# Optimization experiments

Hardware: AMD Instinct MI355X
Metric: run time of the kernel (lower is better)

The kernel has to match this reference:

```python
import jax, jax.numpy as jnp
import numpy as np

B, S, D, H, W = 8, 2048, 128, 8, 64
INT_HEADS = 8          # hardcoded in SpatioTemporalLayer1
EPS_COS = 1e-8
EPS_LN = 1e-5


def _mha(q_in, k_in, v_in, in_w, in_b, out_w, out_b, nh, mask=None):
    # q_in/k_in/v_in: (batch, len, d); torch nn.MultiheadAttention math (eval, no dropout)
    b, lq, d = q_in.shape
    hd = d // nh
    q = (q_in @ in_w[:d].T + in_b[:d]).reshape(b, lq, nh, hd)
    k = (k_in @ in_w[d:2 * d].T + in_b[d:2 * d]).reshape(b, k_in.shape[1], nh, hd)
    v = (v_in @ in_w[2 * d:].T + in_b[2 * d:]).reshape(b, v_in.shape[1], nh, hd)
    scores = jnp.einsum('bihd,bjhd->bhij', q, k) / jnp.sqrt(jnp.asarray(hd, q_in.dtype))
    if mask is not None:
        scores = scores + mask
    attn = jax.nn.softmax(scores, axis=-1)
    out = jnp.einsum('bhij,bjhd->bihd', attn, v).reshape(b, lq, d)
    return out @ out_w.T + out_b


def _layernorm(x, g, b):
    mu = x.mean(-1, keepdims=True)
    var = ((x - mu) ** 2).mean(-1, keepdims=True)
    return (x - mu) * jax.lax.rsqrt(var + EPS_LN) * g + b


def _cos_normalize(e):
    n = jnp.maximum(jnp.linalg.norm(e, axis=-1, keepdims=True), EPS_COS)
    return e / n


def _forward(x, spatial_info, temporal_info,
             lw_in_w, lw_in_b, lw_out_w, lw_out_b,
             spat_w, spat_b, temp_w, temp_b,
             int_in_w, int_in_b, int_out_w, int_out_b,
             ffn_w1, ffn_b1, ffn_w2, ffn_b2,
             ln1_g, ln1_b, ln2_g, ln2_b):
    b, s, d = x.shape
    # --- local window attention (S % W == 0 here, so no padding path) ---
    nw = s // W
    xw = x.reshape(b * nw, W, d)
    causal = jnp.triu(jnp.full((W, W), -jnp.inf, x.dtype), k=1)
    attn = _mha(xw, xw, xw, lw_in_w, lw_in_b, lw_out_w, lw_out_b, H, causal).reshape(b, s, d)
    x = _layernorm(attn + x, ln1_g, ln1_b)
    # --- FFN (torch nn.GELU default = exact erf) ---
    h = jax.nn.gelu(x @ ffn_w1.T + ffn_b1, approximate=False)
    x = _layernorm(h @ ffn_w2.T + ffn_b2 + x, ln2_g, ln2_b)
    # --- spatio-temporal interaction ---
    se = spatial_info @ spat_w.T + spat_b
    te = temporal_info @ temp_w.T + temp_b
    sn = _cos_normalize(se)
    tn = _cos_normalize(te)
    ss = jnp.einsum('bid,bjd->bij', sn, sn)   # (B,S,S) spatial cosine sim
    ts = jnp.einsum('bid,bjd->bij', tn, tn)   # (B,S,S) temporal cosine sim
    # interaction MHA is batch_first=False: it treats (B,S,D) as (len=B, batch=S, d).
    # Equivalent batch-first call on swapped axes (faithful to the torch source).
    inter = jnp.swapaxes(
        _mha(jnp.swapaxes(se, 0, 1), jnp.swapaxes(te, 0, 1), jnp.swapaxes(te, 0, 1),
             int_in_w, int_in_b, int_out_w, int_out_b, INT_HEADS), 0, 1)
    # similarity[b,i,j,d] = ss[b,i,j]*ts[b,i,j]*inter[b,i,d]; mean over j factorizes:
    sim = (ss * ts).mean(axis=2)              # (B,S)
    return x + sim[..., None] * inter


def setup_inputs() -> dict:
    key = jax.random.key(0)
    ks = jax.random.split(key, 24)
    sc = 0.02
    inp = {
        'x': jax.random.normal(ks[0], (B, S, D), jnp.float32),
        'spatial_info': jax.random.normal(ks[1], (B, S, D), jnp.float32),
        'temporal_info': jax.random.normal(ks[2], (B, S, D), jnp.float32),
        'lw_in_w': jax.random.normal(ks[3], (3 * D, D), jnp.float32) * sc,
        'lw_in_b': jnp.zeros((3 * D,), jnp.float32),
        'lw_out_w': jax.random.normal(ks[4], (D, D), jnp.float32) * sc,
        'lw_out_b': jnp.zeros((D,), jnp.float32),
        'spat_w': jax.random.normal(ks[5], (D, D), jnp.float32) * sc,
        'spat_b': jnp.zeros((D,), jnp.float32),
        'temp_w': jax.random.normal(ks[6], (D, D), jnp.float32) * sc,
        'temp_b': jnp.zeros((D,), jnp.float32),
        'int_in_w': jax.random.normal(ks[7], (3 * D, D), jnp.float32) * sc,
        'int_in_b': jnp.zeros((3 * D,), jnp.float32),
        'int_out_w': jax.random.normal(ks[8], (D, D), jnp.float32) * sc,
        'int_out_b': jnp.zeros((D,), jnp.float32),
        'ffn_w1': jax.random.normal(ks[9], (4 * D, D), jnp.float32) * sc,
        'ffn_b1': jnp.zeros((4 * D,), jnp.float32),
        'ffn_w2': jax.random.normal(ks[10], (D, 4 * D), jnp.float32) * sc,
        'ffn_b2': jnp.zeros((D,), jnp.float32),
        'ln1_g': jnp.ones((D,), jnp.float32),
        'ln1_b': jnp.zeros((D,), jnp.float32),
        'ln2_g': jnp.ones((D,), jnp.float32),
        'ln2_b': jnp.zeros((D,), jnp.float32),
    }
    return inp


def reference(x, spatial_info, temporal_info,
              lw_in_w, lw_in_b, lw_out_w, lw_out_b,
              spat_w, spat_b, temp_w, temp_b,
              int_in_w, int_in_b, int_out_w, int_out_b,
              ffn_w1, ffn_b1, ffn_w2, ffn_b2,
              ln1_g, ln1_b, ln2_g, ln2_b):
    return _forward(x, spatial_info, temporal_info,
                    lw_in_w, lw_in_b, lw_out_w, lw_out_b,
                    spat_w, spat_b, temp_w, temp_b,
                    int_in_w, int_in_b, int_out_w, int_out_b,
                    ffn_w1, ffn_b1, ffn_w2, ffn_b2,
                    ln1_g, ln1_b, ln2_g, ln2_b)
```

## Files before the change

### kernel.cpp

```cpp
#include <hip/hip_runtime.h>
#include <math.h>

#define BB 8
#define SS 2048
#define NTOK (BB * SS)

using bf16x8 = __attribute__((ext_vector_type(8))) short;
using f32x4  = __attribute__((ext_vector_type(4))) float;

__device__ __forceinline__ float gelu_tanh(float x) {
    float y = 0.7978845608f * (x + 0.044715f * x * x * x);
    float e = __expf(2.0f * y);
    float t = 1.0f - 2.0f / (e + 1.0f);
    return 0.5f * x * (1.0f + t);
}
__device__ __forceinline__ unsigned short f2b(float f) {
    unsigned int u = __float_as_uint(f);
    u += 0x7FFFu + ((u >> 16) & 1u);
    return (unsigned short)(u >> 16);
}
__device__ __forceinline__ float b2f(unsigned short u) {
    return __uint_as_float((unsigned int)u << 16);
}
__device__ __forceinline__ bf16x8 ldg_f32_b8(const float* p) {
    float4 f0 = *(const float4*)p, f1 = *(const float4*)(p + 4);
    union { ushort4 u[2]; bf16x8 v; } r;
    r.u[0] = (ushort4){f2b(f0.x), f2b(f0.y), f2b(f0.z), f2b(f0.w)};
    r.u[1] = (ushort4){f2b(f1.x), f2b(f1.y), f2b(f1.z), f2b(f1.w)};
    return r.v;
}

__global__ __launch_bounds__(256) void phase0(
    const float* __restrict__ x,
    const float* __restrict__ lw_in_w, const float* __restrict__ b_in,
    const float* __restrict__ lw_out_w,
    const float* __restrict__ spat_w, const float* __restrict__ temp_w,
    const float* __restrict__ ffn_w1, const float* __restrict__ ffn_w2,
    const float* __restrict__ int_in_w, const float* __restrict__ int_out_w,
    const float* __restrict__ spatial, const float* __restrict__ temporal,
    unsigned short* __restrict__ Wlwob, unsigned short* __restrict__ Wstb,
    unsigned short* __restrict__ Wb,
    unsigned short* __restrict__ Wib, unsigned short* __restrict__ Wiob,
    unsigned short* __restrict__ spb, unsigned short* __restrict__ tpb,
    unsigned short* __restrict__ qkvb,
    float* __restrict__ Mf)
{
    const int tid = threadIdx.x;
    if (blockIdx.x < 256) {
        const int m0 = blockIdx.x * 64;
        const int wv = tid >> 6, lane = tid & 63, ln = lane & 15, q = lane >> 4;
        const int wm = (wv >> 1) * 32, wn = (wv & 1) * 64;
        bf16x8 afr[4][2];
        #pragma unroll
        for (int kf = 0; kf < 4; ++kf)
            #pragma unroll
            for (int fm = 0; fm < 2; ++fm)
                afr[kf][fm] = ldg_f32_b8(x + (size_t)(m0 + wm + fm * 16 + ln) * 128 + kf * 32 + q * 8);
        #pragma unroll
        for (int p = 0; p < 3; ++p) {
            f32x4 acc[2][4] = {};
            #pragma unroll
            for (int kf = 0; kf < 4; ++kf) {
                bf16x8 b[4];
                #pragma unroll
                for (int fn = 0; fn < 4; ++fn)
                    b[fn] = ldg_f32_b8(lw_in_w + (size_t)(p * 128 + wn + fn * 16 + ln) * 128 + kf * 32 + q * 8);
                #pragma unroll
                for (int fm = 0; fm < 2; ++fm)
                    #pragma unroll
                    for (int fn = 0; fn < 4; ++fn)
                        acc[fm][fn] = __builtin_amdgcn_mfma_f32_16x16x32_bf16(afr[kf][fm], b[fn], acc[fm][fn], 0, 0, 0);
            }
            #pragma unroll
            for (int fm = 0; fm < 2; ++fm)
                #pragma unroll
                for (int r = 0; r < 4; ++r) {
                    int rl = wm + fm * 16 + q * 4 + r;
                    #pragma unroll
                    for (int fn = 0; fn < 4; ++fn) {
                        int col = wn + fn * 16 + ln;
                        qkvb[(size_t)(m0 + rl) * 384 + p * 128 + col] =
                            f2b(acc[fm][fn][r] + b_in[p * 128 + col]);
                    }
                }
        }
        return;
    }
    int v = (blockIdx.x - 256) * 256 + tid;
    if (v < 61440) {
        const float* src; unsigned short* dst; int off;
        if (v < 4096)       { src = lw_out_w;  dst = Wlwob;         off = v; }
        else if (v < 8192)  { src = spat_w;    dst = Wstb;          off = v - 4096; }
        else if (v < 12288) { src = temp_w;    dst = Wstb + 16384;  off = v - 8192; }
        else if (v < 28672) { src = ffn_w1;    dst = Wb;            off = v - 12288; }
        else if (v < 45056) { src = ffn_w2;    dst = Wb + 65536;    off = v - 28672; }
        else if (v < 57344) { src = int_in_w;  dst = Wib;           off = v - 45056; }
        else                { src = int_out_w; dst = Wiob;          off = v - 57344; }
        float4 f = *(const float4*)(src + (size_t)off * 4);
        *(ushort4*)(dst + (size_t)off * 4) =
            (ushort4){f2b(f.x), f2b(f.y), f2b(f.z), f2b(f.w)};
    } else if (v < 94208) {
        *(float4*)(Mf + (size_t)(v - 61440) * 4) = (float4){0.f, 0.f, 0.f, 0.f};
    } else {
        int u = v - 94208;
        const float* src; unsigned short* dst;
        if (u < 524288) { src = spatial;  dst = spb; }
        else            { src = temporal; dst = tpb; u -= 524288; }
        float4 f = *(const float4*)(src + (size_t)u * 4);
        *(ushort4*)(dst + (size_t)u * 4) =
            (ushort4){f2b(f.x), f2b(f.y), f2b(f.z), f2b(f.w)};
    }
}

__global__ __launch_bounds__(256) void phase1(
    const float* __restrict__ x,
    const unsigned short* __restrict__ qkvb,
    const unsigned short* __restrict__ lwoutb,
    const float* __restrict__ b_out,
    const float* __restrict__ lng, const float* __restrict__ lnb,
    float* __restrict__ x1, unsigned short* __restrict__ x1b,
    const unsigned short* __restrict__ spb, const unsigned short* __restrict__ tpb,
    const unsigned short* __restrict__ spwb, const unsigned short* __restrict__ tpwb,
    const float* __restrict__ bsp, const float* __restrict__ btp,
    unsigned short* __restrict__ snb, unsigned short* __restrict__ tnb,
    unsigned short* __restrict__ seb, unsigned short* __restrict__ teb)
{
    __shared__ unsigned short Qs[64 * 136];
    __shared__ unsigned short Ks[64 * 136];
    __shared__ unsigned short Vt[128 * 72];
    __shared__ unsigned short Pb[4][32 * 72];
    __shared__ float red[2][128][2];
    const int tid = threadIdx.x;
    const int wv = tid >> 6, lane = tid & 63, ln = lane & 15, q = lane >> 4;

    if (blockIdx.x >= 256) {
        const int idx2 = blockIdx.x - 256;
        const int y = idx2 >> 7;
        const int m0 = (idx2 & 127) * 128;
        const unsigned short* Ab = y ? tpb : spb;
        const unsigned short* Wfb = y ? tpwb : spwb;
        const float* bias = y ? btp : bsp;
        unsigned short* nb = y ? tnb : snb;
        unsigned short* raw = y ? teb : seb;
        const int wm = (wv >> 1) * 64, wn = (wv & 1) * 64;

        f32x4 acc[4][4] = {};
        #pragma unroll
        for (int kf = 0; kf < 4; ++kf) {
            bf16x8 a[4], b[4];
            #pragma unroll
            for (int fm = 0; fm < 4; ++fm)
                a[fm] = *(const bf16x8*)&Ab[(size_t)(m0 + wm + fm * 16 + ln) * 128 + kf * 32 + q * 8];
            #pragma unroll
            for (int fn = 0; fn < 4; ++fn)
                b[fn] = *(const bf16x8*)&Wfb[(size_t)(wn + fn * 16 + ln) * 128 + kf * 32 + q * 8];
            #pragma unroll
            for (int fm = 0; fm < 4; ++fm)
                #pragma unroll
                for (int fn = 0; fn < 4; ++fn)
                    acc[fm][fn] = __builtin_amdgcn_mfma_f32_16x16x32_bf16(a[fm], b[fn], acc[fm][fn], 0, 0, 0);
        }
        #pragma unroll
        for (int fm = 0; fm < 4; ++fm)
            #pragma unroll
            for (int r = 0; r < 4; ++r) {
                int rl = wm + fm * 16 + q * 4 + r;
                float s2 = 0.0f;
                #pragma unroll
                for (int fn = 0; fn < 4; ++fn) {
                    int col = wn + fn * 16 + ln;
                    float vv = acc[fm][fn][r] + bias[col];
                    acc[fm][fn][r] = vv;
                    s2 += vv * vv;
                }
                #pragma unroll
                for (int off = 1; off < 16; off <<= 1) s2 += __shfl_xor(s2, off, 64);
                if (ln == 0) red[0][rl][wv & 1] = s2;
            }
        __syncthreads();
        #pragma unroll
        for (int fm = 0; fm < 4; ++fm)
            #pragma unroll
            for (int r = 0; r < 4; ++r) {
                int rl = wm + fm * 16 + q * 4 + r;
                int row = m0 + rl;
                float inv = 1.0f / fmaxf(sqrtf(red[0][rl][0] + red[0][rl][1]), 1e-8f);
                #pragma unroll
                for (int fn = 0; fn < 4; ++fn) {
                    int col = wn + fn * 16 + ln;
                    float vv = acc[fm][fn][r];
                    nb[(size_t)row * 128 + col] = f2b(vv * inv);
                    raw[(size_t)row * 128 + col] = f2b(vv);
                }
            }
        return;
    }

    const int m0 = blockIdx.x * 64;
    const int wm = (wv >> 1) * 32, wn = (wv & 1) * 64;

    {
        const unsigned short* qrow = qkvb + (size_t)m0 * 384;
        #pragma unroll
        for (int t = 0; t < 12; ++t) {
            int idx = tid + t * 256;
            int r = idx / 48, c = (idx % 48) * 8;
            uint4 vv = *(const uint4*)&qrow[(size_t)r * 384 + c];
            if (c < 128)      *(uint4*)&Qs[r * 136 + c] = vv;
            else if (c < 256) *(uint4*)&Ks[r * 136 + (c - 128)] = vv;
            else {
                const unsigned short* pv = (const unsigned short*)&vv;
                #pragma unroll
                for (int c2 = 0; c2 < 8; ++c2)
                    Vt[(c - 256 + c2) * 72 + r] = pv[c2];
            }
        }
    }
    __syncthreads();

    {
        const int mh = wv >> 1, hq = wv & 1;
        unsigned short* P = &Pb[wv][0];
        #pragma unroll
        for (int hh = 0; hh < 4; ++hh) {
            const int h = hq * 4 + hh;
            f32x4 sacc[2][4] = {};
            bf16x8 az[2] = {}, bz[4] = {};
            if (q < 2) {
                #pragma unroll
                for (int fm = 0; fm < 2; ++fm)
                    az[fm] = *(const bf16x8*)&Qs[(mh * 32 + fm * 16 + ln) * 136 + h * 16 + q * 8];
                #pragma unroll
                for (int fn = 0; fn < 4; ++fn)
                    bz[fn] = *(const bf16x8*)&Ks[(fn * 16 + ln) * 136 + h * 16 + q * 8];
            }
            #pragma unroll
            for (int fm = 0; fm < 2; ++fm)
                #pragma unroll
                for (int fn = 0; fn < 4; ++fn)
                    sacc[fm][fn] = __builtin_amdgcn_mfma_f32_16x16x32_bf16(az[fm], bz[fn], sacc[fm][fn], 0, 0, 0);
            float invr[2][4];
            #pragma unroll
            for (int fm = 0; fm < 2; ++fm)
                #pragma unroll
                for (int r = 0; r < 4; ++r) {
                    int gi = mh * 32 + fm * 16 + q * 4 + r;
                    float mx = -1e30f;
                    #pragma unroll
                    for (int fn = 0; fn < 4; ++fn) {
                        int j = fn * 16 + ln;
                        float s = sacc[fm][fn][r] * 0.25f;
                        if (j > gi) s = -1e30f;
                        sacc[fm][fn][r] = s;
                        mx = fmaxf(mx, s);
                    }
                    #pragma unroll
                    for (int off = 1; off < 16; off <<= 1)
                        mx = fmaxf(mx, __shfl_xor(mx, off, 64));
                    float sum = 0.0f;
                    #pragma unroll
                    for (int fn = 0; fn < 4; ++fn) {
                        float p_ = __expf(sacc[fm][fn][r] - mx);
                        sacc[fm][fn][r] = p_;
                        sum += p_;
                    }
                    #pragma unroll
                    for (int off = 1; off < 16; off <<= 1)
                        sum += __shfl_xor(sum, off, 64);
                    invr[fm][r] = 1.0f / sum;
                    #pragma unroll
                    for (int fn = 0; fn < 4; ++fn)
                        P[(fm * 16 + q * 4 + r) * 72 + fn * 16 + ln] = f2b(sacc[fm][fn][r]);
                }
            f32x4 oacc[2] = {};
            #pragma unroll
            for (int kf2 = 0; kf2 < 2; ++kf2) {
                bf16x8 pa[2], vb;
                #pragma unroll
                for (int fm = 0; fm < 2; ++fm)
                    pa[fm] = *(const bf16x8*)&P[(fm * 16 + ln) * 72 + kf2 * 32 + q * 8];
                vb = *(const bf16x8*)&Vt[(h * 16 + ln) * 72 + kf2 * 32 + q * 8];
                #pragma unroll
                for (int fm = 0; fm < 2; ++fm)
                    oacc[fm] = __builtin_amdgcn_mfma_f32_16x16x32_bf16(pa[fm], vb, oacc[fm], 0, 0, 0);
            }
            #pragma unroll
            for (int fm = 0; fm < 2; ++fm)
                #pragma unroll
                for (int r = 0; r < 4; ++r)
                    Qs[(mh * 32 + fm * 16 + q * 4 + r) * 136 + h * 16 + ln] =
                        f2b(oacc[fm][r] * invr[fm][r]);
        }
    }
    __syncthreads();

    f32x4 acc[2][4] = {};
    #pragma unroll
    for (int kf = 0; kf < 4; ++kf) {
        bf16x8 a[2], b[4];
        #pragma unroll
        for (int fm = 0; fm < 2; ++fm)
            a[fm] = *(const bf16x8*)&Qs[(wm + fm * 16 + ln) * 136 + kf * 32 + q * 8];
        #pragma unroll
        for (int fn = 0; fn < 4; ++fn)
            b[fn] = *(const bf16x8*)&lwoutb[(size_t)(wn + fn * 16 + ln) * 128 + kf * 32 + q * 8];
        #pragma unroll
        for (int fm = 0; fm < 2; ++fm)
            #pragma unroll
            for (int fn = 0; fn < 4; ++fn)
                acc[fm][fn] = __builtin_amdgcn_mfma_f32_16x16x32_bf16(a[fm], b[fn], acc[fm][fn], 0, 0, 0);
    }
    #pragma unroll
    for (int fm = 0; fm < 2; ++fm)
        #pragma unroll
        for (int r = 0; r < 4; ++r) {
            int rl = wm + fm * 16 + q * 4 + r;
            int row = m0 + rl;
            float s1 = 0.0f, s2 = 0.0f;
            #pragma unroll
            for (int fn = 0; fn < 4; ++fn) {
                int col = wn + fn * 16 + ln;
                float vv = acc[fm][fn][r] + b_out[col] + x[(size_t)row * 128 + col];
                acc[fm][fn][r] = vv;
                s1 += vv; s2 += vv * vv;
            }
            #pragma unroll
            for (int off = 1; off < 16; off <<= 1) {
                s1 += __shfl_xor(s1, off, 64);
                s2 += __shfl_xor(s2, off, 64);
            }
            if (ln == 0) { red[0][rl][wv & 1] = s1; red[1][rl][wv & 1] = s2; }
        }
    __syncthreads();
    #pragma unroll
    for (int fm = 0; fm < 2; ++fm)
        #pragma unroll
        for (int r = 0; r < 4; ++r) {
            int rl = wm + fm * 16 + q * 4 + r;
            int row = m0 + rl;
            float mu = (red[0][rl][0] + red[0][rl][1]) * (1.0f / 128.0f);
            float var = (red[1][rl][0] + red[1][rl][1]) * (1.0f / 128.0f) - mu * mu;
            float rs = rsqrtf(var + 1e-5f);
            #pragma unroll
            for (int fn = 0; fn < 4; ++fn) {
                int col = wn + fn * 16 + ln;
                float o = (acc[fm][fn][r] - mu) * rs * lng[col] + lnb[col];
                x1[(size_t)row * 128 + col] = o;
                x1b[(size_t)row * 128 + col] = f2b(o);
            }
        }
}

__global__ __launch_bounds__(256) void phase2(
    const unsigned short* __restrict__ x1b, const float* __restrict__ x1,
    const unsigned short* __restrict__ Wb,
    const float* __restrict__ b1, const float* __restrict__ b2,
    const float* __restrict__ lng, const float* __restrict__ lnb,
    float* __restrict__ x2,
    const unsigned short* __restrict__ snb, const unsigned short* __restrict__ tnb,
    float* __restrict__ Mf)
{
    __shared__ __align__(16) char pool[34816];
    const int tid = threadIdx.x;
    const int wv = tid >> 6, lane = tid & 63, ln = lane & 15, q = lane >> 4;

    if (blockIdx.x < 512) {
        unsigned short* Hw = (unsigned short*)pool + wv * 1152;
        float* part = (float*)(pool + 9216);
        const int t0 = blockIdx.x * 32;
        const int rg = wv & 1, hh = wv >> 1;
        const int r0 = t0 + rg * 16;
        const unsigned short* w1 = Wb;
        const unsigned short* w2 = Wb + 65536;

        bf16x8 afr[4];
        #pragma unroll
        for (int kf = 0; kf < 4; ++kf)
            afr[kf] = *(const bf16x8*)&x1b[(size_t)(r0 + ln) * 128 + kf * 32 + q * 8];

        f32x4 acc2[8] = {};
        #pragma unroll
        for (int ch = 0; ch < 4; ++ch) {
            const int hc0 = (hh * 4 + ch) * 64;
            f32x4 acc1[4] = {};
            #pragma unroll
            for (int kf = 0; kf < 4; ++kf) {
                bf16x8 b[4];
                #pragma unroll
                for (int fn = 0; fn < 4; ++fn)
                    b[fn] = *(const bf16x8*)&w1[(size_t)(hc0 + fn * 16 + ln) * 128 + kf * 32 + q * 8];
                #pragma unroll
                for (int fn = 0; fn < 4; ++fn)
                    acc1[fn] = __builtin_amdgcn_mfma_f32_16x16x32_bf16(afr[kf], b[fn], acc1[fn], 0, 0, 0);
            }
            #pragma unroll
            for (int fn = 0; fn < 4; ++fn)
                #pragma unroll
                for (int r = 0; r < 4; ++r)
                    Hw[(q * 4 + r) * 72 + fn * 16 + ln] =
                        f2b(gelu_tanh(acc1[fn][r] + b1[hc0 + fn * 16 + ln]));
            #pragma unroll
            for (int kf2 = 0; kf2 < 2; ++kf2) {
                bf16x8 a = *(const bf16x8*)&Hw[ln * 72 + kf2 * 32 + q * 8];
                bf16x8 b8[8];
                #pragma unroll
                for (int fn = 0; fn < 8; ++fn)
                    b8[fn] = *(const bf16x8*)&w2[(size_t)(fn * 16 + ln) * 512 + hc0 + kf2 * 32 + q * 8];
                #pragma unroll
                for (int fn = 0; fn < 8; ++fn)
                    acc2[fn] = __builtin_amdgcn_mfma_f32_16x16x32_bf16(a, b8[fn], acc2[fn], 0, 0, 0);
            }
        }
        float* pw = part + rg * 2112;
        if (hh == 1) {
            #pragma unroll
            for (int fn = 0; fn < 8; ++fn)
                #pragma unroll
                for (int r = 0; r < 4; ++r)
                    pw[(q * 4 + r) * 132 + fn * 16 + ln] = acc2[fn][r];
        }
        __syncthreads();
        if (hh == 1) return;
        #pragma unroll
        for (int r = 0; r < 4; ++r) {
            int row = r0 + q * 4 + r;
            float s1 = 0.0f, s2 = 0.0f;
            #pragma unroll
            for (int fn = 0; fn < 8; ++fn) {
                int col = fn * 16 + ln;
                float vv = acc2[fn][r] + pw[(q * 4 + r) * 132 + col]
                         + b2[col] + x1[(size_t)row * 128 + col];
                acc2[fn][r] = vv;
                s1 += vv; s2 += vv * vv;
            }
            #pragma unroll
            for (int off = 1; off < 16; off <<= 1) {
                s1 += __shfl_xor(s1, off, 64);
                s2 += __shfl_xor(s2, off, 64);
            }
            float mu = s1 * (1.0f / 128.0f);
            float var = s2 * (1.0f / 128.0f) - mu * mu;
            float rs = rsqrtf(var + 1e-5f);
            #pragma unroll
            for (int fn = 0; fn < 8; ++fn) {
                int col = fn * 16 + ln;
                x2[(size_t)row * 128 + col] = (acc2[fn][r] - mu) * rs * lng[col] + lnb[col];
            }
        }
        return;
    }

    {
        unsigned short* Sst = (unsigned short*)pool;
        unsigned short* Tst = (unsigned short*)(pool + 17408);
        const int idx2 = blockIdx.x - 512;
        const int d0 = (idx2 & 1) * 64, e0 = ((idx2 >> 1) & 1) * 64;
        const int z = idx2 >> 2;
        const int b = z >> 4, chunk = z & 15;
        const size_t rowb = (size_t)(b * SS + chunk * 128);

        #pragma unroll
        for (int it = 0; it < 4; ++it) {
            int j = (tid & 31) + it * 32;
            int c8 = (tid >> 5) * 8;
            uint4 sv = *(const uint4*)&snb[(rowb + j) * 128 + d0 + c8];
            uint4 tv = *(const uint4*)&tnb[(rowb + j) * 128 + e0 + c8];
            const unsigned short* sp = (const unsigned short*)&sv;
            const unsigned short* tp = (const unsigned short*)&tv;
            #pragma unroll
            for (int c = 0; c < 8; ++c) {
                Sst[(c8 + c) * 136 + j] = sp[c];
                Tst[(c8 + c) * 136 + j] = tp[c];
            }
        }
        __syncthreads();

        const int wm = (wv >> 1) * 32, wn = (wv & 1) * 32;
        f32x4 acc[2][2] = {};
        #pragma unroll
        for (int kf = 0; kf < 4; ++kf) {
            bf16x8 a[2], bb[2];
            #pragma unroll
            for (int fm = 0; fm < 2; ++fm)
                a[fm] = *(const bf16x8*)&Tst[(wm + fm * 16 + ln) * 136 + kf * 32 + q * 8];
            #pragma unroll
            for (int fn = 0; fn < 2; ++fn)
                bb[fn] = *(const bf16x8*)&Sst[(wn + fn * 16 + ln) * 136 + kf * 32 + q * 8];
            #pragma unroll
            for (int fm = 0; fm < 2; ++fm)
                #pragma unroll
                for (int fn = 0; fn < 2; ++fn)
                    acc[fm][fn] = __builtin_amdgcn_mfma_f32_16x16x32_bf16(a[fm], bb[fn], acc[fm][fn], 0, 0, 0);
        }
        float* pp = Mf + (size_t)b * 16384;
        #pragma unroll
        for (int fm = 0; fm < 2; ++fm)
            #pragma unroll
            for (int r = 0; r < 4; ++r) {
                int ee = e0 + wm + fm * 16 + q * 4 + r;
                #pragma unroll
                for (int fn = 0; fn < 2; ++fn) {
                    int dd = d0 + wn + fn * 16 + ln;
                    unsafeAtomicAdd(&pp[(size_t)ee * 128 + dd], acc[fm][fn][r]);
                }
            }
    }
}

__global__ __launch_bounds__(256) void simgemm_kernel(
    const unsigned short* __restrict__ snb, const unsigned short* __restrict__ tnb,
    const float* __restrict__ Mf, float* __restrict__ sim)
{
    __shared__ float red[64][2];
    const int tid = threadIdx.x, m0 = blockIdx.x * 64, b = m0 >> 11;
    const int wv = tid >> 6, lane = tid & 63, ln = lane & 15, q = lane >> 4;
    const int wm = (wv >> 1) * 32, wn = (wv & 1) * 64;

    f32x4 acc[2][4] = {};
    #pragma unroll
    for (int kf = 0; kf < 4; ++kf) {
        bf16x8 a[2], bb[4];
        #pragma unroll
        for (int fm = 0; fm < 2; ++fm)
            a[fm] = *(const bf16x8*)&snb[(size_t)(m0 + wm + fm * 16 + ln) * 128 + kf * 32 + q * 8];
        #pragma unroll
        for (int fn = 0; fn < 4; ++fn)
            bb[fn] = ldg_f32_b8(Mf + (size_t)b * 16384 + (size_t)(wn + fn * 16 + ln) * 128 + kf * 32 + q * 8);
        #pragma unroll
        for (int fm = 0; fm < 2; ++fm)
            #pragma unroll
            for (int fn = 0; fn < 4; ++fn)
                acc[fm][fn] = __builtin_amdgcn_mfma_f32_16x16x32_bf16(a[fm], bb[fn], acc[fm][fn], 0, 0, 0);
    }
    #pragma unroll
    for (int fm = 0; fm < 2; ++fm)
        #pragma unroll
        for (int r = 0; r < 4; ++r) {
            int rl = wm + fm * 16 + q * 4 + r;
            int row = m0 + rl;
            float s = 0.0f;
            #pragma unroll
            for (int fn = 0; fn < 4; ++fn) {
                int col = wn + fn * 16 + ln;
                s += acc[fm][fn][r] * b2f(tnb[(size_t)row * 128 + col]);
            }
            #pragma unroll
            for (int off = 1; off < 16; off <<= 1) s += __shfl_xor(s, off, 64);
            if (ln == 0) red[rl][wv & 1] = s;
        }
    __syncthreads();
    if (tid < 64) sim[m0 + tid] = (red[tid][0] + red[tid][1]) * (1.0f / (float)SS);
}

__global__ __launch_bounds__(256) void inter_block(
    const unsigned short* __restrict__ seb, const unsigned short* __restrict__ teb,
    const unsigned short* __restrict__ Wib,
    const float* __restrict__ b_int,
    const unsigned short* __restrict__ Wiob,
    const float* __restrict__ b_io,
    const float* __restrict__ sim, const float* __restrict__ x2,
    float* __restrict__ out)
{
    __shared__ unsigned short Qs[64 * 136];
    __shared__ unsigned short KVs[64 * 256];
    const int tid = threadIdx.x, s0 = blockIdx.x * 8;
    const int wv = tid >> 6, lane = tid & 63, ln = lane & 15, q = lane >> 4;
    const int wm = (wv >> 1) * 32, wn = (wv & 1) * 64;

    bf16x8 afr[4][2];
    #pragma unroll
    for (int kf = 0; kf < 4; ++kf)
        #pragma unroll
        for (int fm = 0; fm < 2; ++fm) {
            int rl = wm + fm * 16 + ln;
            size_t g = (size_t)(rl >> 3) * 2048 + s0 + (rl & 7);
            afr[kf][fm] = *(const bf16x8*)&seb[g * 128 + kf * 32 + q * 8];
        }

    #pragma unroll
    for (int p = 0; p < 3; ++p) {
        if (p == 1) {
            #pragma unroll
            for (int kf = 0; kf < 4; ++kf)
                #pragma unroll
                for (int fm = 0; fm < 2; ++fm) {
                    int rl = wm + fm * 16 + ln;
                    size_t g = (size_t)(rl >> 3) * 2048 + s0 + (rl & 7);
                    afr[kf][fm] = *(const bf16x8*)&teb[g * 128 + kf * 32 + q * 8];
                }
        }
        f32x4 acc[2][4] = {};
        #pragma unroll
        for (int kf = 0; kf < 4; ++kf) {
            bf16x8 b[4];
            #pragma unroll
            for (int fn = 0; fn < 4; ++fn)
                b[fn] = *(const bf16x8*)&Wib[(size_t)(p * 128 + wn + fn * 16 + ln) * 128 + kf * 32 + q * 8];
            #pragma unroll
            for (int fm = 0; fm < 2; ++fm)
                #pragma unroll
                for (int fn = 0; fn < 4; ++fn)
                    acc[fm][fn] = __builtin_amdgcn_mfma_f32_16x16x32_bf16(afr[kf][fm], b[fn], acc[fm][fn], 0, 0, 0);
        }
        #pragma unroll
        for (int fm = 0; fm < 2; ++fm)
            #pragma unroll
            for (int r = 0; r < 4; ++r) {
                int rl = wm + fm * 16 + q * 4 + r;
                #pragma unroll
                for (int fn = 0; fn < 4; ++fn) {
                    int col = wn + fn * 16 + ln;
                    unsigned short v = f2b(acc[fm][fn][r] + b_int[p * 128 + col]);
                    if (p == 0) Qs[rl * 136 + col] = v;
                    else        KVs[rl * 256 + (p - 1) * 128 + col] = v;
                }
            }
        __syncthreads();
    }

    #pragma unroll
    for (int tt = 0; tt < 2; ++tt) {
        int task = tid + tt * 256;
        int ss = task >> 6, h = (task >> 3) & 7, i = task & 7;
        int rq = i * 8 + ss;
        float qr[16];
        {
            uint4 q0 = *(const uint4*)&Qs[rq * 136 + h * 16];
            uint4 q1 = *(const uint4*)&Qs[rq * 136 + h * 16 + 8];
            const unsigned short* p0 = (const unsigned short*)&q0;
            const unsigned short* p1 = (const unsigned short*)&q1;
            #pragma unroll
            for (int c = 0; c < 8; ++c) { qr[c] = b2f(p0[c]); qr[8 + c] = b2f(p1[c]); }
        }
        float sc[8];
        #pragma unroll
        for (int j = 0; j < 8; ++j) {
            uint4 k0 = *(const uint4*)&KVs[(j * 8 + ss) * 256 + h * 16];
            uint4 k1 = *(const uint4*)&KVs[(j * 8 + ss) * 256 + h * 16 + 8];
            const unsigned short* kp0 = (const unsigned short*)&k0;
            const unsigned short* kp1 = (const unsigned short*)&k1;
            float s = 0.0f;
            #pragma unroll
            for (int c = 0; c < 8; ++c) {
                s = fmaf(qr[c], b2f(kp0[c]), s);
                s = fmaf(qr[8 + c], b2f(kp1[c]), s);
            }
            sc[j] = s * 0.25f;
        }
        float mx = -1e30f;
        #pragma unroll
        for (int j = 0; j < 8; ++j) mx = fmaxf(mx, sc[j]);
        float pe[8], se = 0.0f;
        #pragma unroll
        for (int j = 0; j < 8; ++j) { pe[j] = __expf(sc[j] - mx); se += pe[j]; }
        float inv = 1.0f / se;
        float o[16] = {};
        #pragma unroll
        for (int j = 0; j < 8; ++j) {
            uint4 v0 = *(const uint4*)&KVs[(j * 8 + ss) * 256 + 128 + h * 16];
            uint4 v1 = *(const uint4*)&KVs[(j * 8 + ss) * 256 + 128 + h * 16 + 8];
            const unsigned short* vp0 = (const unsigned short*)&v0;
            const unsigned short* vp1 = (const unsigned short*)&v1;
            #pragma unroll
            for (int c = 0; c < 8; ++c) {
                o[c]     += pe[j] * b2f(vp0[c]);
                o[8 + c] += pe[j] * b2f(vp1[c]);
            }
        }
        ushort4 w0 = (ushort4){f2b(o[0]*inv),  f2b(o[1]*inv),  f2b(o[2]*inv),  f2b(o[3]*inv)};
        ushort4 w1 = (ushort4){f2b(o[4]*inv),  f2b(o[5]*inv),  f2b(o[6]*inv),  f2b(o[7]*inv)};
        ushort4 w2 = (ushort4){f2b(o[8]*inv),  f2b(o[9]*inv),  f2b(o[10]*inv), f2b(o[11]*inv)};
        ushort4 w3 = (ushort4){f2b(o[12]*inv), f2b(o[13]*inv), f2b(o[14]*inv), f2b(o[15]*inv)};
        *(ushort4*)&Qs[rq * 136 + h * 16]      = w0;
        *(ushort4*)&Qs[rq * 136 + h * 16 + 4]  = w1;
        *(ushort4*)&Qs[rq * 136 + h * 16 + 8]  = w2;
        *(ushort4*)&Qs[rq * 136 + h * 16 + 12] = w3;
    }
    __syncthreads();

    f32x4 acc[2][4] = {};
    #pragma unroll
    for (int kf = 0; kf < 4; ++kf) {
        bf16x8 a[2], b[4];
        #pragma unroll
        for (int fm = 0; fm < 2; ++fm)
            a[fm] = *(const bf16x8*)&Qs[(wm + fm * 16 + ln) * 136 + kf * 32 + q * 8];
        #pragma unroll
        for (int fn = 0; fn < 4; ++fn)
            b[fn] = *(const bf16x8*)&Wiob[(size_t)(wn + fn * 16 + ln) * 128 + kf * 32 + q * 8];
        #pragma unroll
        for (int fm = 0; fm < 2; ++fm)
            #pragma unroll
            for (int fn = 0; fn < 4; ++fn)
                acc[fm][fn] = __builtin_amdgcn_mfma_f32_16x16x32_bf16(a[fm], b[fn], acc[fm][fn], 0, 0, 0);
    }
    #pragma unroll
    for (int fm = 0; fm < 2; ++fm)
        #pragma unroll
        for (int r = 0; r < 4; ++r) {
            int rl = wm + fm * 16 + q * 4 + r;
            size_t g = (size_t)(rl >> 3) * 2048 + s0 + (rl & 7);
            float sc = sim[g];
            #pragma unroll
            for (int fn = 0; fn < 4; ++fn) {
                int col = wn + fn * 16 + ln;
                out[g * 128 + col] = (acc[fm][fn][r] + b_io[col]) * sc + x2[g * 128 + col];
            }
        }
}

extern "C" void kernel_launch(void* const* d_in, const int* in_sizes, int n_in,
                              void* d_out, int out_size, void* d_ws, size_t ws_size,
                              hipStream_t stream)
{
    const float* x        = (const float*)d_in[0];
    const float* spatial  = (const float*)d_in[1];
    const float* temporal = (const float*)d_in[2];
    const float* lw_in_w  = (const float*)d_in[3];
    const float* lw_in_b  = (const float*)d_in[4];
    const float* lw_out_w = (const float*)d_in[5];
    const float* lw_out_b = (const float*)d_in[6];
    const float* spat_w   = (const float*)d_in[7];
    const float* spat_b   = (const float*)d_in[8];
    const float* temp_w   = (const float*)d_in[9];
    const float* temp_b   = (const float*)d_in[10];
    const float* int_in_w = (const float*)d_in[11];
    const float* int_in_b = (const float*)d_in[12];
    const float* int_out_w= (const float*)d_in[13];
    const float* int_out_b= (const float*)d_in[14];
    const float* ffn_b1   = (const float*)d_in[16];
    const float* ffn_b2   = (const float*)d_in[18];
    const float* ln1_g    = (const float*)d_in[19];
    const float* ln1_b    = (const float*)d_in[20];
    const float* ln2_g    = (const float*)d_in[21];
    const float* ln2_b    = (const float*)d_in[22];
    float* out = (float*)d_out;

    char* base = (char*)d_ws;
    float*          x1    = (float*)(base + 0);
    unsigned short* x1b   = (unsigned short*)(base + 8388608);
    float*          x2    = (float*)(base + 12582912);
    unsigned short* snb   = (unsigned short*)(base + 20971520);
    unsigned short* tnb   = (unsigned short*)(base + 25165824);
    unsigned short* seb   = (unsigned short*)(base + 29360128);
    unsigned short* teb   = (unsigned short*)(base + 33554432);
    unsigned short* Wb    = (unsigned short*)(base + 37748736);
    unsigned short* Wib   = (unsigned short*)(base + 38010880);
    unsigned short* Wiob  = (unsigned short*)(base + 38109184);
    float*          Mf    = (float*)(base + 38141952);
    float*          simb  = (float*)(base + 38666240);
    unsigned short* Wlwob = (unsigned short*)(base + 38731776);
    unsigned short* Wstb  = (unsigned short*)(base + 38764544);
    unsigned short* spb   = (unsigned short*)(base + 38830080);
    unsigned short* tpb   = (unsigned short*)(base + 43024384);
    unsigned short* qkvb  = (unsigned short*)(base + 47218688);

    phase0<<<4720, 256, 0, stream>>>(
        x, lw_in_w, lw_in_b, lw_out_w, spat_w, temp_w,
        (const float*)d_in[15], (const float*)d_in[17], int_in_w, int_out_w,
        spatial, temporal,
        Wlwob, Wstb, Wb, Wib, Wiob, spb, tpb, qkvb, Mf);
    phase1<<<512, 256, 0, stream>>>(
        x, qkvb, Wlwob, lw_out_b, ln1_g, ln1_b, x1, x1b,
        spb, tpb, Wstb, Wstb + 16384, spat_b, temp_b,
        snb, tnb, seb, teb);
    phase2<<<1024, 256, 0, stream>>>(
        x1b, x1, Wb, ffn_b1, ffn_b2, ln2_g, ln2_b, x2, snb, tnb, Mf);
    simgemm_kernel<<<256, 256, 0, stream>>>(snb, tnb, Mf, simb);
    inter_block<<<256, 256, 0, stream>>>(
        seb, teb, Wib, int_in_b, Wiob, int_out_b, simb, x2, out);
}
```

Before: 225.7 us.

## Replace atomic Mf accumulation with per-group partial buffers reduced in simgemm

The T^T·S cross-product blocks in phase2 previously each covered one 128-row chunk and atomically added into a zeroed Mf buffer. Each block now loops over four chunks, accumulating in registers, and writes its tile to one of four partial buffers with plain stores. simgemm sums the four partials while loading its B operand. This removes the zeroing pass in phase0 and the float atomics, and cuts the phase2 grid from 1024 to 640 blocks. In exchange, each reduction block runs longer and with less parallelism, and simgemm reads four times as much partial data.

```diff
diff --git a/kernel.cpp b/kernel.cpp
--- a/kernel.cpp
+++ b/kernel.cpp
@@ -42,8 +42,7 @@
     unsigned short* __restrict__ Wb,
     unsigned short* __restrict__ Wib, unsigned short* __restrict__ Wiob,
     unsigned short* __restrict__ spb, unsigned short* __restrict__ tpb,
-    unsigned short* __restrict__ qkvb,
-    float* __restrict__ Mf)
+    unsigned short* __restrict__ qkvb)
 {
     const int tid = threadIdx.x;
     if (blockIdx.x < 256) {
@@ -99,10 +98,8 @@
         float4 f = *(const float4*)(src + (size_t)off * 4);
         *(ushort4*)(dst + (size_t)off * 4) =
             (ushort4){f2b(f.x), f2b(f.y), f2b(f.z), f2b(f.w)};
-    } else if (v < 94208) {
-        *(float4*)(Mf + (size_t)(v - 61440) * 4) = (float4){0.f, 0.f, 0.f, 0.f};
     } else {
-        int u = v - 94208;
+        int u = v - 61440;
         const float* src; unsigned short* dst;
         if (u < 524288) { src = spatial;  dst = spb; }
         else            { src = temporal; dst = tpb; u -= 524288; }
@@ -358,7 +355,7 @@
     const float* __restrict__ lng, const float* __restrict__ lnb,
     float* __restrict__ x2,
     const unsigned short* __restrict__ snb, const unsigned short* __restrict__ tnb,
-    float* __restrict__ Mf)
+    float* __restrict__ part)
 {
     __shared__ __align__(16) char pool[34816];
     const int tid = threadIdx.x;
@@ -366,7 +363,7 @@
 
     if (blockIdx.x < 512) {
         unsigned short* Hw = (unsigned short*)pool + wv * 1152;
-        float* part = (float*)(pool + 9216);
+        float* partl = (float*)(pool + 9216);
         const int t0 = blockIdx.x * 32;
         const int rg = wv & 1, hh = wv >> 1;
         const int r0 = t0 + rg * 16;
@@ -411,7 +408,7 @@
                     acc2[fn] = __builtin_amdgcn_mfma_f32_16x16x32_bf16(a, b8[fn], acc2[fn], 0, 0, 0);
             }
         }
-        float* pw = part + rg * 2112;
+        float* pw = partl + rg * 2112;
         if (hh == 1) {
             #pragma unroll
             for (int fn = 0; fn < 8; ++fn)
@@ -456,43 +453,45 @@
         const int idx2 = blockIdx.x - 512;
         const int d0 = (idx2 & 1) * 64, e0 = ((idx2 >> 1) & 1) * 64;
         const int z = idx2 >> 2;
-        const int b = z >> 4, chunk = z & 15;
-        const size_t rowb = (size_t)(b * SS + chunk * 128);
-
-        #pragma unroll
-        for (int it = 0; it < 4; ++it) {
-            int j = (tid & 31) + it * 32;
-            int c8 = (tid >> 5) * 8;
-            uint4 sv = *(const uint4*)&snb[(rowb + j) * 128 + d0 + c8];
-            uint4 tv = *(const uint4*)&tnb[(rowb + j) * 128 + e0 + c8];
-            const unsigned short* sp = (const unsigned short*)&sv;
-            const unsigned short* tp = (const unsigned short*)&tv;
-            #pragma unroll
-            for (int c = 0; c < 8; ++c) {
-                Sst[(c8 + c) * 136 + j] = sp[c];
-                Tst[(c8 + c) * 136 + j] = tp[c];
-            }
-        }
-        __syncthreads();
-
+        const int b = z >> 2, cg = z & 3;
         const int wm = (wv >> 1) * 32, wn = (wv & 1) * 32;
+
         f32x4 acc[2][2] = {};
-        #pragma unroll
-        for (int kf = 0; kf < 4; ++kf) {
-            bf16x8 a[2], bb[2];
-            #pragma unroll
-            for (int fm = 0; fm < 2; ++fm)
-                a[fm] = *(const bf16x8*)&Tst[(wm + fm * 16 + ln) * 136 + kf * 32 + q * 8];
-            #pragma unroll
-            for (int fn = 0; fn < 2; ++fn)
-                bb[fn] = *(const bf16x8*)&Sst[(wn + fn * 16 + ln) * 136 + kf * 32 + q * 8];
-            #pragma unroll
-            for (int fm = 0; fm < 2; ++fm)
+        for (int cc = 0; cc < 4; ++cc) {
+            const size_t rowb = (size_t)(b * SS + (cg * 4 + cc) * 128);
+            #pragma unroll
+            for (int it = 0; it < 4; ++it) {
+                int j = (tid >> 3) + it * 32;
+                int c8 = (tid & 7) * 8;
+                uint4 sv = *(const uint4*)&snb[(rowb + j) * 128 + d0 + c8];
+                uint4 tv = *(const uint4*)&tnb[(rowb + j) * 128 + e0 + c8];
+                const unsigned short* sp = (const unsigned short*)&sv;
+                const unsigned short* tp = (const unsigned short*)&tv;
+                #pragma unroll
+                for (int c = 0; c < 8; ++c) {
+                    Sst[(c8 + c) * 136 + j] = sp[c];
+                    Tst[(c8 + c) * 136 + j] = tp[c];
+                }
+            }
+            __syncthreads();
+            #pragma unroll
+            for (int kf = 0; kf < 4; ++kf) {
+                bf16x8 a[2], bb[2];
+                #pragma unroll
+                for (int fm = 0; fm < 2; ++fm)
+                    a[fm] = *(const bf16x8*)&Tst[(wm + fm * 16 + ln) * 136 + kf * 32 + q * 8];
                 #pragma unroll
                 for (int fn = 0; fn < 2; ++fn)
-                    acc[fm][fn] = __builtin_amdgcn_mfma_f32_16x16x32_bf16(a[fm], bb[fn], acc[fm][fn], 0, 0, 0);
-        }
-        float* pp = Mf + (size_t)b * 16384;
+                    bb[fn] = *(const bf16x8*)&Sst[(wn + fn * 16 + ln) * 136 + kf * 32 + q * 8];
+                #pragma unroll
+                for (int fm = 0; fm < 2; ++fm)
+                    #pragma unroll
+                    for (int fn = 0; fn < 2; ++fn)
+                        acc[fm][fn] = __builtin_amdgcn_mfma_f32_16x16x32_bf16(a[fm], bb[fn], acc[fm][fn], 0, 0, 0);
+            }
+            __syncthreads();
+        }
+        float* pp = part + ((size_t)(cg * 8 + b)) * 16384;
         #pragma unroll
         for (int fm = 0; fm < 2; ++fm)
             #pragma unroll
@@ -501,7 +500,7 @@
                 #pragma unroll
                 for (int fn = 0; fn < 2; ++fn) {
                     int dd = d0 + wn + fn * 16 + ln;
-                    unsafeAtomicAdd(&pp[(size_t)ee * 128 + dd], acc[fm][fn][r]);
+                    pp[(size_t)ee * 128 + dd] = acc[fm][fn][r];
                 }
             }
     }
@@ -509,7 +508,7 @@
 
 __global__ __launch_bounds__(256) void simgemm_kernel(
     const unsigned short* __restrict__ snb, const unsigned short* __restrict__ tnb,
-    const float* __restrict__ Mf, float* __restrict__ sim)
+    const float* __restrict__ part, float* __restrict__ sim)
 {
     __shared__ float red[64][2];
     const int tid = threadIdx.x, m0 = blockIdx.x * 64, b = m0 >> 11;
@@ -524,8 +523,22 @@
         for (int fm = 0; fm < 2; ++fm)
             a[fm] = *(const bf16x8*)&snb[(size_t)(m0 + wm + fm * 16 + ln) * 128 + kf * 32 + q * 8];
         #pragma unroll
-        for (int fn = 0; fn < 4; ++fn)
-            bb[fn] = ldg_f32_b8(Mf + (size_t)b * 16384 + (size_t)(wn + fn * 16 + ln) * 128 + kf * 32 + q * 8);
+        for (int fn = 0; fn < 4; ++fn) {
+            const float* pp = part + (size_t)b * 16384
+                            + (size_t)(wn + fn * 16 + ln) * 128 + kf * 32 + q * 8;
+            float4 f0 = (float4){0.f, 0.f, 0.f, 0.f}, f1 = f0;
+            #pragma unroll
+            for (int cg = 0; cg < 4; ++cg) {
+                const float* ps = pp + (size_t)cg * 131072;
+                float4 a0 = *(const float4*)ps, a1 = *(const float4*)(ps + 4);
+                f0.x += a0.x; f0.y += a0.y; f0.z += a0.z; f0.w += a0.w;
+                f1.x += a1.x; f1.y += a1.y; f1.z += a1.z; f1.w += a1.w;
+            }
+            union { ushort4 u[2]; bf16x8 v; } r_;
+            r_.u[0] = (ushort4){f2b(f0.x), f2b(f0.y), f2b(f0.z), f2b(f0.w)};
+            r_.u[1] = (ushort4){f2b(f1.x), f2b(f1.y), f2b(f1.z), f2b(f1.w)};
+            bb[fn] = r_.v;
+        }
         #pragma unroll
         for (int fm = 0; fm < 2; ++fm)
             #pragma unroll
@@ -747,26 +760,26 @@
     unsigned short* Wb    = (unsigned short*)(base + 37748736);
     unsigned short* Wib   = (unsigned short*)(base + 38010880);
     unsigned short* Wiob  = (unsigned short*)(base + 38109184);
-    float*          Mf    = (float*)(base + 38141952);
     float*          simb  = (float*)(base + 38666240);
     unsigned short* Wlwob = (unsigned short*)(base + 38731776);
     unsigned short* Wstb  = (unsigned short*)(base + 38764544);
     unsigned short* spb   = (unsigned short*)(base + 38830080);
     unsigned short* tpb   = (unsigned short*)(base + 43024384);
     unsigned short* qkvb  = (unsigned short*)(base + 47218688);
-
-    phase0<<<4720, 256, 0, stream>>>(
+    float*          part  = (float*)(base + 59801600);
+
+    phase0<<<4592, 256, 0, stream>>>(
         x, lw_in_w, lw_in_b, lw_out_w, spat_w, temp_w,
         (const float*)d_in[15], (const float*)d_in[17], int_in_w, int_out_w,
         spatial, temporal,
-        Wlwob, Wstb, Wb, Wib, Wiob, spb, tpb, qkvb, Mf);
+        Wlwob, Wstb, Wb, Wib, Wiob, spb, tpb, qkvb);
     phase1<<<512, 256, 0, stream>>>(
         x, qkvb, Wlwob, lw_out_b, ln1_g, ln1_b, x1, x1b,
         spb, tpb, Wstb, Wstb + 16384, spat_b, temp_b,
         snb, tnb, seb, teb);
-    phase2<<<1024, 256, 0, stream>>>(
-        x1b, x1, Wb, ffn_b1, ffn_b2, ln2_g, ln2_b, x2, snb, tnb, Mf);
-    simgemm_kernel<<<256, 256, 0, stream>>>(snb, tnb, Mf, simb);
+    phase2<<<640, 256, 0, stream>>>(
+        x1b, x1, Wb, ffn_b1, ffn_b2, ln2_g, ln2_b, x2, snb, tnb, part);
+    simgemm_kernel<<<256, 256, 0, stream>>>(snb, tnb, part, simb);
     inter_block<<<256, 256, 0, stream>>>(
         seb, teb, Wib, int_in_b, Wiob, int_out_b, simb, x2, out);
 }
```

New measurement: 235.9 us. 1.05x slower.

## Split fused FFN/AtB phase into separate kernels and retile FFN work split

Applied to the files above, without the earlier changes.

Breaks the combined phase2 kernel, which ran FFN blocks and the sn^T·tn reduction blocks side by side, into a dedicated ffn_kernel and a separate atb_kernel launched one after the other. The FFN kernel now gives each block 16 tokens and splits the 512-wide hidden dimension four ways across the waves, combining three partial sums in shared memory; before, each block handled 32 tokens with a two-way hidden split. The aim is more FFN parallelism with less shared memory per block. In exchange there is an extra launch, the two independent workloads no longer overlap, and every weight byte is reloaded for half as many tokens. The Mf accumulator is also moved to a new workspace offset past the qkv buffer.

```diff
diff --git a/kernel.cpp b/kernel.cpp
--- a/kernel.cpp
+++ b/kernel.cpp
@@ -351,160 +351,157 @@
         }
 }
 
-__global__ __launch_bounds__(256) void phase2(
+__global__ __launch_bounds__(256) void ffn_kernel(
     const unsigned short* __restrict__ x1b, const float* __restrict__ x1,
     const unsigned short* __restrict__ Wb,
     const float* __restrict__ b1, const float* __restrict__ b2,
     const float* __restrict__ lng, const float* __restrict__ lnb,
-    float* __restrict__ x2,
+    float* __restrict__ x2)
+{
+    __shared__ unsigned short Hw_s[4][16 * 72];
+    __shared__ float part[3][16][132];
+    const int tid = threadIdx.x;
+    const int wv = tid >> 6, lane = tid & 63, ln = lane & 15, q = lane >> 4;
+    const int t0 = blockIdx.x * 16;
+    const int hh = wv;
+    unsigned short* Hw = Hw_s[wv];
+    const unsigned short* w1 = Wb;
+    const unsigned short* w2 = Wb + 65536;
+
+    bf16x8 afr[4];
+    #pragma unroll
+    for (int kf = 0; kf < 4; ++kf)
+        afr[kf] = *(const bf16x8*)&x1b[(size_t)(t0 + ln) * 128 + kf * 32 + q * 8];
+
+    f32x4 acc2[8] = {};
+    #pragma unroll
+    for (int ch = 0; ch < 2; ++ch) {
+        const int hc0 = (hh * 2 + ch) * 64;
+        f32x4 acc1[4] = {};
+        #pragma unroll
+        for (int kf = 0; kf < 4; ++kf) {
+            bf16x8 b[4];
+            #pragma unroll
+            for (int fn = 0; fn < 4; ++fn)
+                b[fn] = *(const bf16x8*)&w1[(size_t)(hc0 + fn * 16 + ln) * 128 + kf * 32 + q * 8];
+            #pragma unroll
+            for (int fn = 0; fn < 4; ++fn)
+                acc1[fn] = __builtin_amdgcn_mfma_f32_16x16x32_bf16(afr[kf], b[fn], acc1[fn], 0, 0, 0);
+        }
+        #pragma unroll
+        for (int fn = 0; fn < 4; ++fn)
+            #pragma unroll
+            for (int r = 0; r < 4; ++r)
+                Hw[(q * 4 + r) * 72 + fn * 16 + ln] =
+                    f2b(gelu_tanh(acc1[fn][r] + b1[hc0 + fn * 16 + ln]));
+        #pragma unroll
+        for (int kf2 = 0; kf2 < 2; ++kf2) {
+            bf16x8 a = *(const bf16x8*)&Hw[ln * 72 + kf2 * 32 + q * 8];
+            bf16x8 b8[8];
+            #pragma unroll
+            for (int fn = 0; fn < 8; ++fn)
+                b8[fn] = *(const bf16x8*)&w2[(size_t)(fn * 16 + ln) * 512 + hc0 + kf2 * 32 + q * 8];
+            #pragma unroll
+            for (int fn = 0; fn < 8; ++fn)
+                acc2[fn] = __builtin_amdgcn_mfma_f32_16x16x32_bf16(a, b8[fn], acc2[fn], 0, 0, 0);
+        }
+    }
+    if (hh != 0) {
+        #pragma unroll
+        for (int fn = 0; fn < 8; ++fn)
+            #pragma unroll
+            for (int r = 0; r < 4; ++r)
+                part[hh - 1][q * 4 + r][fn * 16 + ln] = acc2[fn][r];
+    }
+    __syncthreads();
+    if (hh != 0) return;
+    #pragma unroll
+    for (int r = 0; r < 4; ++r) {
+        int row = t0 + q * 4 + r;
+        float s1 = 0.0f, s2 = 0.0f;
+        #pragma unroll
+        for (int fn = 0; fn < 8; ++fn) {
+            int col = fn * 16 + ln;
+            float vv = acc2[fn][r] + part[0][q * 4 + r][col] + part[1][q * 4 + r][col]
+                     + part[2][q * 4 + r][col] + b2[col] + x1[(size_t)row * 128 + col];
+            acc2[fn][r] = vv;
+            s1 += vv; s2 += vv * vv;
+        }
+        #pragma unroll
+        for (int off = 1; off < 16; off <<= 1) {
+            s1 += __shfl_xor(s1, off, 64);
+            s2 += __shfl_xor(s2, off, 64);
+        }
+        float mu = s1 * (1.0f / 128.0f);
+        float var = s2 * (1.0f / 128.0f) - mu * mu;
+        float rs = rsqrtf(var + 1e-5f);
+        #pragma unroll
+        for (int fn = 0; fn < 8; ++fn) {
+            int col = fn * 16 + ln;
+            x2[(size_t)row * 128 + col] = (acc2[fn][r] - mu) * rs * lng[col] + lnb[col];
+        }
+    }
+}
+
+__global__ __launch_bounds__(256) void atb_kernel(
     const unsigned short* __restrict__ snb, const unsigned short* __restrict__ tnb,
     float* __restrict__ Mf)
 {
-    __shared__ __align__(16) char pool[34816];
+    __shared__ __align__(16) unsigned short Sst[64 * 136];
+    __shared__ __align__(16) unsigned short Tst[64 * 136];
     const int tid = threadIdx.x;
     const int wv = tid >> 6, lane = tid & 63, ln = lane & 15, q = lane >> 4;
-
-    if (blockIdx.x < 512) {
-        unsigned short* Hw = (unsigned short*)pool + wv * 1152;
-        float* part = (float*)(pool + 9216);
-        const int t0 = blockIdx.x * 32;
-        const int rg = wv & 1, hh = wv >> 1;
-        const int r0 = t0 + rg * 16;
-        const unsigned short* w1 = Wb;
-        const unsigned short* w2 = Wb + 65536;
-
-        bf16x8 afr[4];
-        #pragma unroll
-        for (int kf = 0; kf < 4; ++kf)
-            afr[kf] = *(const bf16x8*)&x1b[(size_t)(r0 + ln) * 128 + kf * 32 + q * 8];
-
-        f32x4 acc2[8] = {};
-        #pragma unroll
-        for (int ch = 0; ch < 4; ++ch) {
-            const int hc0 = (hh * 4 + ch) * 64;
-            f32x4 acc1[4] = {};
-            #pragma unroll
-            for (int kf = 0; kf < 4; ++kf) {
-                bf16x8 b[4];
-                #pragma unroll
-                for (int fn = 0; fn < 4; ++fn)
-                    b[fn] = *(const bf16x8*)&w1[(size_t)(hc0 + fn * 16 + ln) * 128 + kf * 32 + q * 8];
-                #pragma unroll
-                for (int fn = 0; fn < 4; ++fn)
-                    acc1[fn] = __builtin_amdgcn_mfma_f32_16x16x32_bf16(afr[kf], b[fn], acc1[fn], 0, 0, 0);
-            }
-            #pragma unroll
-            for (int fn = 0; fn < 4; ++fn)
-                #pragma unroll
-                for (int r = 0; r < 4; ++r)
-                    Hw[(q * 4 + r) * 72 + fn * 16 + ln] =
-                        f2b(gelu_tanh(acc1[fn][r] + b1[hc0 + fn * 16 + ln]));
-            #pragma unroll
-            for (int kf2 = 0; kf2 < 2; ++kf2) {
-                bf16x8 a = *(const bf16x8*)&Hw[ln * 72 + kf2 * 32 + q * 8];
-                bf16x8 b8[8];
-                #pragma unroll
-                for (int fn = 0; fn < 8; ++fn)
-                    b8[fn] = *(const bf16x8*)&w2[(size_t)(fn * 16 + ln) * 512 + hc0 + kf2 * 32 + q * 8];
-                #pragma unroll
-                for (int fn = 0; fn < 8; ++fn)
-                    acc2[fn] = __builtin_amdgcn_mfma_f32_16x16x32_bf16(a, b8[fn], acc2[fn], 0, 0, 0);
-            }
-        }
-        float* pw = part + rg * 2112;
-        if (hh == 1) {
-            #pragma unroll
-            for (int fn = 0; fn < 8; ++fn)
-                #pragma unroll
-                for (int r = 0; r < 4; ++r)
-                    pw[(q * 4 + r) * 132 + fn * 16 + ln] = acc2[fn][r];
-        }
-        __syncthreads();
-        if (hh == 1) return;
+    const int idx2 = blockIdx.x;
+    const int d0 = (idx2 & 1) * 64, e0 = ((idx2 >> 1) & 1) * 64;
+    const int z = idx2 >> 2;
+    const int b = z >> 4, chunk = z & 15;
+    const size_t rowb = (size_t)(b * SS + chunk * 128);
+
+    #pragma unroll
+    for (int it = 0; it < 4; ++it) {
+        int j = (tid & 31) + it * 32;
+        int c8 = (tid >> 5) * 8;
+        uint4 sv = *(const uint4*)&snb[(rowb + j) * 128 + d0 + c8];
+        uint4 tv = *(const uint4*)&tnb[(rowb + j) * 128 + e0 + c8];
+        const unsigned short* sp = (const unsigned short*)&sv;
+        const unsigned short* tp = (const unsigned short*)&tv;
+        #pragma unroll
+        for (int c = 0; c < 8; ++c) {
+            Sst[(c8 + c) * 136 + j] = sp[c];
+            Tst[(c8 + c) * 136 + j] = tp[c];
+        }
+    }
+    __syncthreads();
+
+    const int wm = (wv >> 1) * 32, wn = (wv & 1) * 32;
+    f32x4 acc[2][2] = {};
+    #pragma unroll
+    for (int kf = 0; kf < 4; ++kf) {
+        bf16x8 a[2], bb[2];
+        #pragma unroll
+        for (int fm = 0; fm < 2; ++fm)
+            a[fm] = *(const bf16x8*)&Tst[(wm + fm * 16 + ln) * 136 + kf * 32 + q * 8];
+        #pragma unroll
+        for (int fn = 0; fn < 2; ++fn)
+            bb[fn] = *(const bf16x8*)&Sst[(wn + fn * 16 + ln) * 136 + kf * 32 + q * 8];
+        #pragma unroll
+        for (int fm = 0; fm < 2; ++fm)
+            #pragma unroll
+            for (int fn = 0; fn < 2; ++fn)
+                acc[fm][fn] = __builtin_amdgcn_mfma_f32_16x16x32_bf16(a[fm], bb[fn], acc[fm][fn], 0, 0, 0);
+    }
+    float* pp = Mf + (size_t)b * 16384;
+    #pragma unroll
+    for (int fm = 0; fm < 2; ++fm)
         #pragma unroll
         for (int r = 0; r < 4; ++r) {
-            int row = r0 + q * 4 + r;
-            float s1 = 0.0f, s2 = 0.0f;
-            #pragma unroll
-            for (int fn = 0; fn < 8; ++fn) {
-                int col = fn * 16 + ln;
-                float vv = acc2[fn][r] + pw[(q * 4 + r) * 132 + col]
-                         + b2[col] + x1[(size_t)row * 128 + col];
-                acc2[fn][r] = vv;
-                s1 += vv; s2 += vv * vv;
-            }
-            #pragma unroll
-            for (int off = 1; off < 16; off <<= 1) {
-                s1 += __shfl_xor(s1, off, 64);
-                s2 += __shfl_xor(s2, off, 64);
-            }
-            float mu = s1 * (1.0f / 128.0f);
-            float var = s2 * (1.0f / 128.0f) - mu * mu;
-            float rs = rsqrtf(var + 1e-5f);
-            #pragma unroll
-            for (int fn = 0; fn < 8; ++fn) {
-                int col = fn * 16 + ln;
-                x2[(size_t)row * 128 + col] = (acc2[fn][r] - mu) * rs * lng[col] + lnb[col];
-            }
-        }
-        return;
-    }
-
-    {
-        unsigned short* Sst = (unsigned short*)pool;
-        unsigned short* Tst = (unsigned short*)(pool + 17408);
-        const int idx2 = blockIdx.x - 512;
-        const int d0 = (idx2 & 1) * 64, e0 = ((idx2 >> 1) & 1) * 64;
-        const int z = idx2 >> 2;
-        const int b = z >> 4, chunk = z & 15;
-        const size_t rowb = (size_t)(b * SS + chunk * 128);
-
-        #pragma unroll
-        for (int it = 0; it < 4; ++it) {
-            int j = (tid & 31) + it * 32;
-            int c8 = (tid >> 5) * 8;
-            uint4 sv = *(const uint4*)&snb[(rowb + j) * 128 + d0 + c8];
-            uint4 tv = *(const uint4*)&tnb[(rowb + j) * 128 + e0 + c8];
-            const unsigned short* sp = (const unsigned short*)&sv;
-            const unsigned short* tp = (const unsigned short*)&tv;
-            #pragma unroll
-            for (int c = 0; c < 8; ++c) {
-                Sst[(c8 + c) * 136 + j] = sp[c];
-                Tst[(c8 + c) * 136 + j] = tp[c];
-            }
-        }
-        __syncthreads();
-
-        const int wm = (wv >> 1) * 32, wn = (wv & 1) * 32;
-        f32x4 acc[2][2] = {};
-        #pragma unroll
-        for (int kf = 0; kf < 4; ++kf) {
-            bf16x8 a[2], bb[2];
-            #pragma unroll
-            for (int fm = 0; fm < 2; ++fm)
-                a[fm] = *(const bf16x8*)&Tst[(wm + fm * 16 + ln) * 136 + kf * 32 + q * 8];
-            #pragma unroll
-            for (int fn = 0; fn < 2; ++fn)
-                bb[fn] = *(const bf16x8*)&Sst[(wn + fn * 16 + ln) * 136 + kf * 32 + q * 8];
-            #pragma unroll
-            for (int fm = 0; fm < 2; ++fm)
-                #pragma unroll
-                for (int fn = 0; fn < 2; ++fn)
-                    acc[fm][fn] = __builtin_amdgcn_mfma_f32_16x16x32_bf16(a[fm], bb[fn], acc[fm][fn], 0, 0, 0);
-        }
-        float* pp = Mf + (size_t)b * 16384;
-        #pragma unroll
-        for (int fm = 0; fm < 2; ++fm)
-            #pragma unroll
-            for (int r = 0; r < 4; ++r) {
-                int ee = e0 + wm + fm * 16 + q * 4 + r;
-                #pragma unroll
-                for (int fn = 0; fn < 2; ++fn) {
-                    int dd = d0 + wn + fn * 16 + ln;
-                    unsafeAtomicAdd(&pp[(size_t)ee * 128 + dd], acc[fm][fn][r]);
-                }
-            }
-    }
+            int ee = e0 + wm + fm * 16 + q * 4 + r;
+            #pragma unroll
+            for (int fn = 0; fn < 2; ++fn) {
+                int dd = d0 + wn + fn * 16 + ln;
+                unsafeAtomicAdd(&pp[(size_t)ee * 128 + dd], acc[fm][fn][r]);
+            }
+        }
 }
 
 __global__ __launch_bounds__(256) void simgemm_kernel(
@@ -747,13 +744,13 @@
     unsigned short* Wb    = (unsigned short*)(base + 37748736);
     unsigned short* Wib   = (unsigned short*)(base + 38010880);
     unsigned short* Wiob  = (unsigned short*)(base + 38109184);
-    float*          Mf    = (float*)(base + 38141952);
     float*          simb  = (float*)(base + 38666240);
     unsigned short* Wlwob = (unsigned short*)(base + 38731776);
     unsigned short* Wstb  = (unsigned short*)(base + 38764544);
     unsigned short* spb   = (unsigned short*)(base + 38830080);
     unsigned short* tpb   = (unsigned short*)(base + 43024384);
     unsigned short* qkvb  = (unsigned short*)(base + 47218688);
+    float*          Mf    = (float*)(base + 59801600);
 
     phase0<<<4720, 256, 0, stream>>>(
         x, lw_in_w, lw_in_b, lw_out_w, spat_w, temp_w,
@@ -764,8 +761,9 @@
         x, qkvb, Wlwob, lw_out_b, ln1_g, ln1_b, x1, x1b,
         spb, tpb, Wstb, Wstb + 16384, spat_b, temp_b,
         snb, tnb, seb, teb);
-    phase2<<<1024, 256, 0, stream>>>(
-        x1b, x1, Wb, ffn_b1, ffn_b2, ln2_g, ln2_b, x2, snb, tnb, Mf);
+    ffn_kernel<<<1024, 256, 0, stream>>>(
+        x1b, x1, Wb, ffn_b1, ffn_b2, ln2_g, ln2_b, x2);
+    atb_kernel<<<512, 256, 0, stream>>>(snb, tnb, Mf);
     simgemm_kernel<<<256, 256, 0, stream>>>(snb, tnb, Mf, simb);
     inter_block<<<256, 256, 0, stream>>>(
         seb, teb, Wib, int_in_b, Wiob, int_out_b, simb, x2, out);
```

After: 232.7 us. +3.1%, slower.
